# Kernel optimization log

Measured on AMD Instinct MI355X. Metric: run time of the kernel, lower is better.

## Reference

```python
import jax, jax.numpy as jnp
import numpy as np

N, E, D, H = 50000, 500000, 128, 4
FH = D // H  # per-head dim of gat1
NEG_SLOPE = 0.2
EPS = 1e-16  # PyG softmax denominator epsilon


def _gat_layer(x, src, dst, W, a_src, a_dst, bias, heads, fh):
    # W: [D_in, heads*fh]; a_src/a_dst: [heads, fh]; bias: [heads*fh]
    n = x.shape[0]
    xp = (x @ W).reshape(n, heads, fh)                     # [N,H,F]
    alpha_s = jnp.einsum('nhf,hf->nh', xp, a_src)          # [N,H]
    alpha_d = jnp.einsum('nhf,hf->nh', xp, a_dst)
    e = alpha_s[src] + alpha_d[dst]                        # [E,H]
    e = jnp.where(e > 0, e, NEG_SLOPE * e)                 # leaky_relu
    # edge softmax grouped by destination node
    m = jax.lax.stop_gradient(jax.ops.segment_max(e, dst, num_segments=n))
    a = jnp.exp(e - m[dst])
    denom = jax.ops.segment_sum(a, dst, num_segments=n)
    a = a / (denom[dst] + EPS)                             # [E,H]
    msg = a[:, :, None] * xp[src]                          # [E,H,F]
    out = jax.ops.segment_sum(msg, dst, num_segments=n)    # [N,H,F]
    return out.reshape(n, heads * fh) + bias


def setup_inputs() -> dict:
    key = jax.random.key(0)
    ks = jax.random.split(key, 20)

    def glorot(k, shape):
        fan_in, fan_out = shape[0], shape[-1]
        std = (2.0 / (fan_in + fan_out)) ** 0.5
        return std * jax.random.normal(k, shape, dtype=jnp.float32)

    inp = {
        'x': jax.random.normal(ks[0], (N, 1), dtype=jnp.float32),
        'edge_index': jax.random.randint(ks[1], (E, 2), 0, N, dtype=jnp.int64 if jax.config.jax_enable_x64 else jnp.int32),
        'W_emb': glorot(ks[2], (1, D)),   # nn.Linear(1, d_node), stored as [in,out]
        'b_emb': jnp.zeros((D,), jnp.float32),
        # gat1: in=D, heads=H, per-head out=FH
        'W1': glorot(ks[3], (D, H * FH)),
        'as1': glorot(ks[4], (H, FH)),
        'ad1': glorot(ks[5], (H, FH)),
        'b1': jnp.zeros((H * FH,), jnp.float32),
        # gat2/3/4: in=D, heads=1, out=D
        'W2': glorot(ks[6], (D, D)), 'as2': glorot(ks[7], (1, D)), 'ad2': glorot(ks[8], (1, D)), 'b2': jnp.zeros((D,), jnp.float32),
        'W3': glorot(ks[9], (D, D)), 'as3': glorot(ks[10], (1, D)), 'ad3': glorot(ks[11], (1, D)), 'b3': jnp.zeros((D,), jnp.float32),
        'W4': glorot(ks[12], (D, D)), 'as4': glorot(ks[13], (1, D)), 'ad4': glorot(ks[14], (1, D)), 'b4': jnp.zeros((D,), jnp.float32),
    }
    return inp


def reference(x, edge_index, W_emb, b_emb, W1, as1, ad1, b1,
              W2, as2, ad2, b2, W3, as3, ad3, b3, W4, as4, ad4, b4):
    # emb: Linear(1 -> D)
    h = x @ W_emb + b_emb                                  # [N,D]
    # edge_index.t(): row 0 = src, row 1 = dst; GATConv adds self-loops
    loop = jnp.arange(N, dtype=edge_index.dtype)
    src = jnp.concatenate([edge_index[:, 0], loop])
    dst = jnp.concatenate([edge_index[:, 1], loop])
    h = jax.nn.relu(_gat_layer(h, src, dst, W1, as1, ad1, b1, H, FH))
    h = jax.nn.relu(_gat_layer(h, src, dst, W2, as2, ad2, b2, 1, D))
    h = jax.nn.relu(_gat_layer(h, src, dst, W3, as3, ad3, b3, 1, D))
    h = _gat_layer(h, src, dst, W4, as4, ad4, b4, 1, D)
    return h
```

## Files before the change

kernel.cpp:

```cpp
#include <hip/hip_runtime.h>
#include <math.h>


#define LEAKY(e) ((e) > 0.f ? (e) : 0.2f * (e))

typedef __attribute__((ext_vector_type(8))) short bf16x8;
typedef __attribute__((ext_vector_type(4))) float f32x4;

__device__ inline ushort f32_to_bf16_rne(float f) {
    unsigned u = __float_as_uint(f);
    unsigned r = (u + 0x7FFFu + ((u >> 16) & 1u)) >> 16;
    return (ushort)r;
}
__device__ inline float bf16_to_f32(ushort h) { return __uint_as_float((unsigned)h << 16); }
__device__ inline unsigned pack2(float a, float b) {
    return (unsigned)f32_to_bf16_rne(a) | ((unsigned)f32_to_bf16_rne(b) << 16);
}


__global__ void k_scatterpad(const int* __restrict__ ei, int E, int N,
                             int* __restrict__ deg, int* __restrict__ csr_pad,
                             int* __restrict__ ovf_cnt, int2* __restrict__ ovf,
                             int ovf_cap) {
    int e = blockIdx.x * blockDim.x + threadIdx.x;
    int Et = E + N;
    if (e >= Et) return;
    int src, dst;
    if (e < E) { int2 p = ((const int2*)ei)[e]; src = p.x; dst = p.y; }
    else { src = dst = e - E; }
    int pos = atomicAdd(&deg[dst], 1);
    if (pos < 64) {
        csr_pad[(dst << 6) + pos] = src;
    } else {
        int o = atomicAdd(ovf_cnt, 1);
        if (o < ovf_cap) ovf[o] = make_int2(dst, src);
    }
}


__global__ void k_prep(const float* __restrict__ Wa, const float* __restrict__ Wb,
                       const float* __restrict__ Wc,
                       const float* __restrict__ asa, const float* __restrict__ asb,
                       const float* __restrict__ asc,
                       const float* __restrict__ ada, const float* __restrict__ adb,
                       const float* __restrict__ adc,
                       const float* __restrict__ W_emb, const float* __restrict__ b_emb,
                       const float* __restrict__ W1g, const float* __restrict__ as1g,
                       const float* __restrict__ ad1g,
                       ushort* __restrict__ hi0, ushort* __restrict__ lo0,
                       ushort* __restrict__ hi1, ushort* __restrict__ lo1,
                       ushort* __restrict__ hi2, ushort* __restrict__ lo2,
                       float* __restrict__ was0, float* __restrict__ was1,
                       float* __restrict__ was2,
                       float* __restrict__ wad0, float* __restrict__ wad1,
                       float* __restrict__ wad2,
                       float* __restrict__ consts) {
    __shared__ float su[128], sv[128];
    int b = blockIdx.x, tid = threadIdx.x;
    if (b < 192) {
        int l = b >> 6;
        int idx = (b & 63) * 256 + tid;
        const float* W = (l == 0) ? Wa : (l == 1) ? Wb : Wc;
        ushort* ph = (l == 0) ? hi0 : (l == 1) ? hi1 : hi2;
        ushort* pl = (l == 0) ? lo0 : (l == 1) ? lo1 : lo2;
        int k = idx >> 7, c = idx & 127;
        float w = W[idx];
        ushort hi = f32_to_bf16_rne(w);
        ushort lo = f32_to_bf16_rne(w - bf16_to_f32(hi));
        ph[c * 128 + k] = hi;
        pl[c * 128 + k] = lo;
    } else if (b < 195) {
        if (tid >= 128) return;
        int l = b - 192;
        const float* W  = (l == 0) ? Wa : (l == 1) ? Wb : Wc;
        const float* av = (l == 0) ? asa : (l == 1) ? asb : asc;
        const float* dv = (l == 0) ? ada : (l == 1) ? adb : adc;
        float* ws = (l == 0) ? was0 : (l == 1) ? was1 : was2;
        float* wd = (l == 0) ? wad0 : (l == 1) ? wad1 : wad2;
        int k = tid;
        float s = 0.f, d = 0.f;
        for (int c = 0; c < 128; c++) {
            float w = W[k * 128 + c];
            s += w * av[c];
            d += w * dv[c];
        }
        ws[k] = s; wd[k] = d;
    } else {
        if (tid >= 128) return;
        int f = tid;
        float u = 0.f, v = 0.f;
        for (int k = 0; k < 128; k++) {
            u += W_emb[k] * W1g[k * 128 + f];
            v += b_emb[k] * W1g[k * 128 + f];
        }
        su[f] = u; sv[f] = v;
        consts[f] = u; consts[128 + f] = v;
        __syncthreads();
        if (f < 4) {
            float P = 0.f, Q = 0.f, R = 0.f, S = 0.f;
            for (int j = 0; j < 32; j++) {
                float uu = su[f * 32 + j], vv = sv[f * 32 + j];
                float a = as1g[f * 32 + j], d = ad1g[f * 32 + j];
                P += uu * a; Q += vv * a; R += uu * d; S += vv * d;
            }
            consts[256 + f] = P; consts[260 + f] = Q;
            consts[264 + f] = R; consts[268 + f] = S;
        }
    }
}

__global__ __launch_bounds__(256) void k_l1(const float* __restrict__ x,
        const int* __restrict__ deg, const int* __restrict__ csr_pad,
        const int* __restrict__ ovf_cnt, const int2* __restrict__ ovf,
        const float* __restrict__ consts, const float* __restrict__ b1,
        const float* __restrict__ was2, const float* __restrict__ wad2,
        float* __restrict__ hout, float* __restrict__ a_s, float* __restrict__ a_d, int n) {
    __shared__ float sm[64][4], smw[64][4];
    int tid = threadIdx.x;
    int nl = tid >> 2, q = tid & 3;
    int node = blockIdx.x * 64 + nl;
    bool valid = node < n;
    float P = consts[256 + q], Q = consts[260 + q];
    float R = consts[264 + q], Sc = consts[268 + q];
    float den = 0.f, S = 0.f;
    if (valid) {
        float xd = x[node];
        float c0 = xd * R + Sc + Q;
        int dg = deg[node];
        int dlim = min(dg, 64);
        for (int i = 0; i < dlim; i++) {
            float xs = x[csr_pad[(node << 6) + i]];
            float e = xs * P + c0;
            e = LEAKY(e);
            float w = __expf(e);
            den += w;
            S += w * xs;
        }
        if (dg > 64) {
            int no = *ovf_cnt;
            for (int i = 0; i < no; i++) {
                int2 p = ovf[i];
                if (p.x == node) {
                    float xs = x[p.y];
                    float e = xs * P + c0;
                    e = LEAKY(e);
                    float w = __expf(e);
                    den += w;
                    S += w * xs;
                }
            }
        }
    }
    float inv = 1.f / (den + 1e-16f);
    sm[nl][q] = S * inv;
    smw[nl][q] = den * inv;
    __syncthreads();
    float Sn = sm[nl][q], Swn = smw[nl][q];
    float ps = 0.f, pd = 0.f;
    if (valid) {
#pragma unroll
        for (int j = 0; j < 8; j++) {
            int f = q * 32 + j * 4;
            float4 u = *(const float4*)(consts + f);
            float4 v = *(const float4*)(consts + 128 + f);
            float4 b = *(const float4*)(b1 + f);
            float4 ws = *(const float4*)(was2 + f);
            float4 wd = *(const float4*)(wad2 + f);
            float4 val;
            val.x = fmaxf(Sn * u.x + Swn * v.x + b.x, 0.f);
            val.y = fmaxf(Sn * u.y + Swn * v.y + b.y, 0.f);
            val.z = fmaxf(Sn * u.z + Swn * v.z + b.z, 0.f);
            val.w = fmaxf(Sn * u.w + Swn * v.w + b.w, 0.f);
            *(float4*)(hout + (size_t)node * 128 + f) = val;
            ps += val.x * ws.x + val.y * ws.y + val.z * ws.z + val.w * ws.w;
            pd += val.x * wd.x + val.y * wd.y + val.z * wd.z + val.w * wd.w;
        }
    }
    ps += __shfl_xor(ps, 1, 64); ps += __shfl_xor(ps, 2, 64);
    pd += __shfl_xor(pd, 1, 64); pd += __shfl_xor(pd, 2, 64);
    if (q == 0 && valid) { a_s[node] = ps; a_d[node] = pd; }
}

__global__ __launch_bounds__(256) void k_aggh(const float* __restrict__ h,
        const float* __restrict__ as, const float* __restrict__ ad,
        const int* __restrict__ deg, const int* __restrict__ csr_pad,
        const int* __restrict__ ovf_cnt, const int2* __restrict__ ovf,
        unsigned* __restrict__ aggp, int n) {
    __shared__ int2 s_sw[4][64];
    int w = threadIdx.x >> 6, lane = threadIdx.x & 63;
    int node = blockIdx.x * 4 + w;
    if (node >= n) return;
    int dg = deg[node];
    float adval = ad[node];
    const char* hbase = (const char*)h;

    if (dg <= 64) {
        int boff = 0;
        float e = -INFINITY;
        if (lane < dg) {
            int src = csr_pad[(node << 6) + lane];
            boff = src << 9;
            e = LEAKY(as[src] + adval);
        }
        float m = e;
#pragma unroll
        for (int off = 32; off > 0; off >>= 1) m = fmaxf(m, __shfl_xor(m, off, 64));
        float wt = (lane < dg) ? __expf(e - m) : 0.f;
        float den = wt;
#pragma unroll
        for (int off = 32; off > 0; off >>= 1) den += __shfl_xor(den, off, 64);
        s_sw[w][lane] = make_int2(boff, __float_as_int(wt));
        __builtin_amdgcn_wave_barrier();

        int half = lane >> 5;
        int q16 = (lane & 31) * 16;
        float4 acc = make_float4(0.f, 0.f, 0.f, 0.f);
        int degp = (dg + 7) & ~7;
        for (int j = 0; j < degp; j += 8) {
#pragma unroll
            for (int t = 0; t < 4; t++) {
                int2 p = s_sw[w][j + 2 * t + half];
                float4 v = *(const float4*)(hbase + p.x + q16);
                float wt2 = __int_as_float(p.y);
                acc.x += wt2 * v.x; acc.y += wt2 * v.y;
                acc.z += wt2 * v.z; acc.w += wt2 * v.w;
            }
        }
        acc.x += __shfl_xor(acc.x, 32, 64);
        acc.y += __shfl_xor(acc.y, 32, 64);
        acc.z += __shfl_xor(acc.z, 32, 64);
        acc.w += __shfl_xor(acc.w, 32, 64);
        float inv = 1.f / (den + 1e-16f);
        if (lane < 32) {
            float o0 = acc.x * inv, o1 = acc.y * inv;
            float o2 = acc.z * inv, o3 = acc.w * inv;
            ushort h0 = f32_to_bf16_rne(o0), h1 = f32_to_bf16_rne(o1);
            ushort h2 = f32_to_bf16_rne(o2), h3 = f32_to_bf16_rne(o3);
            uint4 pk;
            pk.x = (unsigned)h0 | ((unsigned)h1 << 16);
            pk.y = pack2(o0 - bf16_to_f32(h0), o1 - bf16_to_f32(h1));
            pk.z = (unsigned)h2 | ((unsigned)h3 << 16);
            pk.w = pack2(o2 - bf16_to_f32(h2), o3 - bf16_to_f32(h3));
            ((uint4*)aggp)[(size_t)node * 32 + lane] = pk;
        }
    } else {
        int lane8 = lane * 8;
        int no = *ovf_cnt;
        int psrc = csr_pad[(node << 6) + lane];
        float m = LEAKY(as[psrc] + adval);
        for (int i = lane; i < no; i += 64) {
            int2 p = ovf[i];
            if (p.x == node) m = fmaxf(m, LEAKY(as[p.y] + adval));
        }
#pragma unroll
        for (int off = 32; off > 0; off >>= 1) m = fmaxf(m, __shfl_xor(m, off, 64));
        float den = 0.f;
        float2 acc = make_float2(0.f, 0.f);
        for (int i = 0; i < 64; i++) {
            int src = csr_pad[(node << 6) + i];
            float e = LEAKY(as[src] + adval);
            float wt = __expf(e - m);
            den += wt;
            float2 v = *(const float2*)(hbase + ((size_t)src << 9) + lane8);
            acc.x += wt * v.x; acc.y += wt * v.y;
        }
        for (int i = 0; i < no; i++) {
            int2 p = ovf[i];
            if (p.x == node) {
                float e = LEAKY(as[p.y] + adval);
                float wt = __expf(e - m);
                den += wt;
                float2 v = *(const float2*)(hbase + ((size_t)p.y << 9) + lane8);
                acc.x += wt * v.x; acc.y += wt * v.y;
            }
        }
        float inv = 1.f / (den + 1e-16f);
        float o0 = acc.x * inv, o1 = acc.y * inv;
        ushort h0 = f32_to_bf16_rne(o0), h1 = f32_to_bf16_rne(o1);
        ((uint2*)aggp)[(size_t)node * 64 + lane] =
            make_uint2((unsigned)h0 | ((unsigned)h1 << 16),
                       pack2(o0 - bf16_to_f32(h0), o1 - bf16_to_f32(h1)));
    }
}

__global__ __launch_bounds__(512) void k_gemm(const uint2* __restrict__ aggp,
        const ushort* __restrict__ wt_hi, const ushort* __restrict__ wt_lo,
        const float* __restrict__ bias, float* __restrict__ hout,
        const float* __restrict__ was_nx, const float* __restrict__ wad_nx,
        float* __restrict__ as_nx, float* __restrict__ ad_nx,
        int n, int do_relu) {
    __shared__ ushort Bh[16 * 128 * 8];
    __shared__ ushort Bl[16 * 128 * 8];
    int tid = threadIdx.x;
#pragma unroll
    for (int rep = 0; rep < 4; rep++) {
        int c = rep * 512 + tid;
        int col = c >> 4, kc = c & 15;
        *(uint4*)(Bh + (size_t)(kc * 128 + col) * 8) = *(const uint4*)(wt_hi + (size_t)col * 128 + kc * 8);
        *(uint4*)(Bl + (size_t)(kc * 128 + col) * 8) = *(const uint4*)(wt_lo + (size_t)col * 128 + kc * 8);
    }
    __syncthreads();

    int wid = tid >> 6, lane = tid & 63;
    int lrow = lane & 15, kgrp = lane >> 4;
    int row_base = blockIdx.x * 128 + wid * 16;

    f32x4 acc[8];
#pragma unroll
    for (int nn = 0; nn < 8; nn++) { acc[nn][0] = 0.f; acc[nn][1] = 0.f; acc[nn][2] = 0.f; acc[nn][3] = 0.f; }

#pragma unroll
    for (int ks = 0; ks < 4; ks++) {
        int kbase = ks * 32 + kgrp * 8;
        int arow = min(row_base + lrow, n - 1);
        const uint2* ap = aggp + (size_t)arow * 64 + (kbase >> 1);
        uint4 q0 = *(const uint4*)ap;
        uint4 q1 = *(const uint4*)(ap + 2);
        int4 hi4 = make_int4(q0.x, q0.z, q1.x, q1.z);
        int4 lo4 = make_int4(q0.y, q0.w, q1.y, q1.w);
        bf16x8 ah = *(bf16x8*)&hi4;
        bf16x8 al = *(bf16x8*)&lo4;
        int kc = ks * 4 + kgrp;
#pragma unroll
        for (int nn = 0; nn < 8; nn++) {
            int col = nn * 16 + lrow;
            bf16x8 bh = *(const bf16x8*)(Bh + (size_t)(kc * 128 + col) * 8);
            bf16x8 bl = *(const bf16x8*)(Bl + (size_t)(kc * 128 + col) * 8);
            acc[nn] = __builtin_amdgcn_mfma_f32_16x16x32_bf16(ah, bh, acc[nn], 0, 0, 0);
            acc[nn] = __builtin_amdgcn_mfma_f32_16x16x32_bf16(ah, bl, acc[nn], 0, 0, 0);
            acc[nn] = __builtin_amdgcn_mfma_f32_16x16x32_bf16(al, bh, acc[nn], 0, 0, 0);
        }
    }

    float bv[8], wsv[8], wdv[8];
#pragma unroll
    for (int nn = 0; nn < 8; nn++) bv[nn] = bias[nn * 16 + lrow];
    if (was_nx) {
#pragma unroll
        for (int nn = 0; nn < 8; nn++) {
            wsv[nn] = was_nx[nn * 16 + lrow];
            wdv[nn] = wad_nx[nn * 16 + lrow];
        }
    }

#pragma unroll
    for (int i = 0; i < 4; i++) {
        int row = row_base + kgrp * 4 + i;
        if (row < n) {
            float ps = 0.f, pd = 0.f;
#pragma unroll
            for (int nn = 0; nn < 8; nn++) {
                float val = acc[nn][i] + bv[nn];
                if (do_relu) val = fmaxf(val, 0.f);
                hout[(size_t)row * 128 + nn * 16 + lrow] = val;
                if (was_nx) { ps += val * wsv[nn]; pd += val * wdv[nn]; }
            }
            if (was_nx) {
#pragma unroll
                for (int off = 1; off < 16; off <<= 1) {
                    ps += __shfl_xor(ps, off, 16);
                    pd += __shfl_xor(pd, off, 16);
                }
                if (lrow == 0) { as_nx[row] = ps; ad_nx[row] = pd; }
            }
        }
    }
}


extern "C" void kernel_launch(void* const* d_in, const int* in_sizes, int n_in,
                              void* d_out, int out_size, void* d_ws, size_t ws_size,
                              hipStream_t stream) {
    const float* x     = (const float*)d_in[0];
    const int*   ei    = (const int*)d_in[1];
    const float* W_emb = (const float*)d_in[2];
    const float* b_emb = (const float*)d_in[3];
    const float* W1g   = (const float*)d_in[4];
    const float* as1g  = (const float*)d_in[5];
    const float* ad1g  = (const float*)d_in[6];
    const float* b1    = (const float*)d_in[7];
    const float* Wl[3]  = {(const float*)d_in[8],  (const float*)d_in[12], (const float*)d_in[16]};
    const float* asl[3] = {(const float*)d_in[9],  (const float*)d_in[13], (const float*)d_in[17]};
    const float* adl[3] = {(const float*)d_in[10], (const float*)d_in[14], (const float*)d_in[18]};
    const float* bl[3]  = {(const float*)d_in[11], (const float*)d_in[15], (const float*)d_in[19]};
    float* out = (float*)d_out;

    int N = in_sizes[0];
    int E = in_sizes[1] / 2;
    int Et = E + N;
    const int OVF_CAP = 65536;

    char* ws = (char*)d_ws;
    size_t off = 0;
    auto alloc = [&](size_t bytes) { size_t p = off; off += (bytes + 255) & ~(size_t)255; return p; };
    int*   deg      = (int*)(ws + alloc((size_t)N * 4));
    int*   ovf_cnt  = (int*)(ws + alloc(4));
    int2*  ovf      = (int2*)(ws + alloc((size_t)OVF_CAP * 8));
    int*   csr_pad  = (int*)(ws + alloc((size_t)N * 64 * 4));
    float* consts   = (float*)(ws + alloc(272 * 4));
    float* a_s0     = (float*)(ws + alloc((size_t)N * 4));
    float* a_d0     = (float*)(ws + alloc((size_t)N * 4));
    float* a_s1     = (float*)(ws + alloc((size_t)N * 4));
    float* a_d1     = (float*)(ws + alloc((size_t)N * 4));
    float* hA       = (float*)(ws + alloc((size_t)N * 128 * 4));
    unsigned* aggp  = (unsigned*)(ws + alloc((size_t)N * 64 * 8));
    ushort* wt_hi[3]; ushort* wt_lo[3];
    float* was[3]; float* wad[3];
    for (int l = 0; l < 3; l++) {
        wt_hi[l] = (ushort*)(ws + alloc(128 * 128 * 2));
        wt_lo[l] = (ushort*)(ws + alloc(128 * 128 * 2));
        was[l]   = (float*)(ws + alloc(128 * 4));
        wad[l]   = (float*)(ws + alloc(128 * 4));
    }

    hipMemsetAsync(deg, 0, (size_t)N * 4, stream);
    hipMemsetAsync(ovf_cnt, 0, 4, stream);
    k_scatterpad<<<(Et + 255) / 256, 256, 0, stream>>>(ei, E, N, deg, csr_pad,
                                                       ovf_cnt, ovf, OVF_CAP);
    k_prep<<<196, 256, 0, stream>>>(Wl[0], Wl[1], Wl[2], asl[0], asl[1], asl[2],
                                    adl[0], adl[1], adl[2],
                                    W_emb, b_emb, W1g, as1g, ad1g,
                                    wt_hi[0], wt_lo[0], wt_hi[1], wt_lo[1], wt_hi[2], wt_lo[2],
                                    was[0], was[1], was[2], wad[0], wad[1], wad[2],
                                    consts);

    k_l1<<<(N + 63) / 64, 256, 0, stream>>>(x, deg, csr_pad, ovf_cnt, ovf, consts, b1,
                                            was[0], wad[0], hA, a_s0, a_d0, N);

    float* as_cur = a_s0; float* ad_cur = a_d0;
    float* as_nxt = a_s1; float* ad_nxt = a_d1;
    for (int l = 0; l < 3; l++) {
        k_aggh<<<(N + 3) / 4, 256, 0, stream>>>(hA, as_cur, ad_cur, deg, csr_pad,
                                                ovf_cnt, ovf, aggp, N);
        if (l < 2) {
            k_gemm<<<(N + 127) / 128, 512, 0, stream>>>((const uint2*)aggp, wt_hi[l], wt_lo[l], bl[l], hA,
                                                        was[l + 1], wad[l + 1], as_nxt, ad_nxt, N, 1);
            float* t;
            t = as_cur; as_cur = as_nxt; as_nxt = t;
            t = ad_cur; ad_cur = ad_nxt; ad_nxt = t;
        } else {
            k_gemm<<<(N + 127) / 128, 512, 0, stream>>>((const uint2*)aggp, wt_hi[l], wt_lo[l], bl[l], out,
                                                        nullptr, nullptr, nullptr, nullptr, N, 0);
        }
    }
}
```

Baseline: 247.7 us.

## Parallelize layer-1 edges across a wavefront, prefetch GEMM A, merge overflow counter

k_l1 now assigns one 64-lane wavefront per node, with 16 lanes per head striding over edges and shuffle reductions. It replaces the old scheme where one thread per head looped serially over every edge. The GEMM kernel issues its A-operand global loads into registers before the LDS barrier, so they overlap with the weight staging. The overflow counter is folded into deg[N], which removes one memset. The trade-offs are more shuffle reductions per node and higher register pressure in the GEMM.

```diff
diff --git a/kernel.cpp b/kernel.cpp
--- a/kernel.cpp
+++ b/kernel.cpp
@@ -20,8 +20,7 @@
 
 __global__ void k_scatterpad(const int* __restrict__ ei, int E, int N,
                              int* __restrict__ deg, int* __restrict__ csr_pad,
-                             int* __restrict__ ovf_cnt, int2* __restrict__ ovf,
-                             int ovf_cap) {
+                             int2* __restrict__ ovf, int ovf_cap) {
     int e = blockIdx.x * blockDim.x + threadIdx.x;
     int Et = E + N;
     if (e >= Et) return;
@@ -32,7 +31,7 @@
     if (pos < 64) {
         csr_pad[(dst << 6) + pos] = src;
     } else {
-        int o = atomicAdd(ovf_cnt, 1);
+        int o = atomicAdd(&deg[N], 1);
         if (o < ovf_cap) ovf[o] = make_int2(dst, src);
     }
 }
@@ -111,80 +110,75 @@
 
 __global__ __launch_bounds__(256) void k_l1(const float* __restrict__ x,
         const int* __restrict__ deg, const int* __restrict__ csr_pad,
-        const int* __restrict__ ovf_cnt, const int2* __restrict__ ovf,
+        const int2* __restrict__ ovf,
         const float* __restrict__ consts, const float* __restrict__ b1,
         const float* __restrict__ was2, const float* __restrict__ wad2,
-        float* __restrict__ hout, float* __restrict__ a_s, float* __restrict__ a_d, int n) {
-    __shared__ float sm[64][4], smw[64][4];
-    int tid = threadIdx.x;
-    int nl = tid >> 2, q = tid & 3;
-    int node = blockIdx.x * 64 + nl;
-    bool valid = node < n;
+        float* __restrict__ hout, float* __restrict__ a_s, float* __restrict__ a_d,
+        int n) {
+    int w = threadIdx.x >> 6, lane = threadIdx.x & 63;
+    int node = blockIdx.x * 4 + w;
+    if (node >= n) return;
+    int q = lane & 3;
+    int el = lane >> 2;
     float P = consts[256 + q], Q = consts[260 + q];
     float R = consts[264 + q], Sc = consts[268 + q];
+    float xd = x[node];
+    float c0 = xd * R + Sc + Q;
+    int dg = deg[node];
+    int dlim = min(dg, 64);
     float den = 0.f, S = 0.f;
-    if (valid) {
-        float xd = x[node];
-        float c0 = xd * R + Sc + Q;
-        int dg = deg[node];
-        int dlim = min(dg, 64);
-        for (int i = 0; i < dlim; i++) {
-            float xs = x[csr_pad[(node << 6) + i]];
-            float e = xs * P + c0;
-            e = LEAKY(e);
-            float w = __expf(e);
-            den += w;
-            S += w * xs;
-        }
-        if (dg > 64) {
-            int no = *ovf_cnt;
-            for (int i = 0; i < no; i++) {
-                int2 p = ovf[i];
-                if (p.x == node) {
-                    float xs = x[p.y];
-                    float e = xs * P + c0;
-                    e = LEAKY(e);
-                    float w = __expf(e);
-                    den += w;
-                    S += w * xs;
-                }
-            }
-        }
+    for (int i = el; i < dlim; i += 16) {
+        float xs = x[csr_pad[(node << 6) + i]];
+        float e = xs * P + c0;
+        e = LEAKY(e);
+        float wgt = __expf(e);
+        den += wgt;
+        S += wgt * xs;
+    }
+    if (dg > 64) {
+        int no = deg[n];
+        for (int i = el; i < no; i += 16) {
+            int2 p = ovf[i];
+            if (p.x == node) {
+                float xs = x[p.y];
+                float e = xs * P + c0;
+                e = LEAKY(e);
+                float wgt = __expf(e);
+                den += wgt;
+                S += wgt * xs;
+            }
+        }
+    }
+#pragma unroll
+    for (int off = 4; off < 64; off <<= 1) {
+        den += __shfl_xor(den, off, 64);
+        S += __shfl_xor(S, off, 64);
     }
     float inv = 1.f / (den + 1e-16f);
-    sm[nl][q] = S * inv;
-    smw[nl][q] = den * inv;
-    __syncthreads();
-    float Sn = sm[nl][q], Swn = smw[nl][q];
-    float ps = 0.f, pd = 0.f;
-    if (valid) {
-#pragma unroll
-        for (int j = 0; j < 8; j++) {
-            int f = q * 32 + j * 4;
-            float4 u = *(const float4*)(consts + f);
-            float4 v = *(const float4*)(consts + 128 + f);
-            float4 b = *(const float4*)(b1 + f);
-            float4 ws = *(const float4*)(was2 + f);
-            float4 wd = *(const float4*)(wad2 + f);
-            float4 val;
-            val.x = fmaxf(Sn * u.x + Swn * v.x + b.x, 0.f);
-            val.y = fmaxf(Sn * u.y + Swn * v.y + b.y, 0.f);
-            val.z = fmaxf(Sn * u.z + Swn * v.z + b.z, 0.f);
-            val.w = fmaxf(Sn * u.w + Swn * v.w + b.w, 0.f);
-            *(float4*)(hout + (size_t)node * 128 + f) = val;
-            ps += val.x * ws.x + val.y * ws.y + val.z * ws.z + val.w * ws.w;
-            pd += val.x * wd.x + val.y * wd.y + val.z * wd.z + val.w * wd.w;
-        }
-    }
-    ps += __shfl_xor(ps, 1, 64); ps += __shfl_xor(ps, 2, 64);
-    pd += __shfl_xor(pd, 1, 64); pd += __shfl_xor(pd, 2, 64);
-    if (q == 0 && valid) { a_s[node] = ps; a_d[node] = pd; }
+    float Sn = S * inv, Swn = den * inv;
+    int f = q * 32 + el * 2;
+    float2 u  = *(const float2*)(consts + f);
+    float2 v  = *(const float2*)(consts + 128 + f);
+    float2 bb = *(const float2*)(b1 + f);
+    float2 ws = *(const float2*)(was2 + f);
+    float2 wd = *(const float2*)(wad2 + f);
+    float v0 = fmaxf(Sn * u.x + Swn * v.x + bb.x, 0.f);
+    float v1 = fmaxf(Sn * u.y + Swn * v.y + bb.y, 0.f);
+    *(float2*)(hout + (size_t)node * 128 + f) = make_float2(v0, v1);
+    float ps = v0 * ws.x + v1 * ws.y;
+    float pd = v0 * wd.x + v1 * wd.y;
+#pragma unroll
+    for (int off = 1; off < 64; off <<= 1) {
+        ps += __shfl_xor(ps, off, 64);
+        pd += __shfl_xor(pd, off, 64);
+    }
+    if (lane == 0) { a_s[node] = ps; a_d[node] = pd; }
 }
 
 __global__ __launch_bounds__(256) void k_aggh(const float* __restrict__ h,
         const float* __restrict__ as, const float* __restrict__ ad,
         const int* __restrict__ deg, const int* __restrict__ csr_pad,
-        const int* __restrict__ ovf_cnt, const int2* __restrict__ ovf,
+        const int2* __restrict__ ovf,
         unsigned* __restrict__ aggp, int n) {
     __shared__ int2 s_sw[4][64];
     int w = threadIdx.x >> 6, lane = threadIdx.x & 63;
@@ -245,7 +239,7 @@
         }
     } else {
         int lane8 = lane * 8;
-        int no = *ovf_cnt;
+        int no = deg[n];
         int psrc = csr_pad[(node << 6) + lane];
         float m = LEAKY(as[psrc] + adval);
         for (int i = lane; i < no; i += 64) {
@@ -299,11 +293,20 @@
         *(uint4*)(Bh + (size_t)(kc * 128 + col) * 8) = *(const uint4*)(wt_hi + (size_t)col * 128 + kc * 8);
         *(uint4*)(Bl + (size_t)(kc * 128 + col) * 8) = *(const uint4*)(wt_lo + (size_t)col * 128 + kc * 8);
     }
-    __syncthreads();
 
     int wid = tid >> 6, lane = tid & 63;
     int lrow = lane & 15, kgrp = lane >> 4;
     int row_base = blockIdx.x * 128 + wid * 16;
+    int arow = min(row_base + lrow, n - 1);
+
+    const uint4* ap = (const uint4*)(aggp + (size_t)arow * 64);
+    uint4 qa[8];
+#pragma unroll
+    for (int ks = 0; ks < 4; ks++) {
+        qa[2 * ks]     = ap[ks * 8 + kgrp * 2];
+        qa[2 * ks + 1] = ap[ks * 8 + kgrp * 2 + 1];
+    }
+    __syncthreads();
 
     f32x4 acc[8];
 #pragma unroll
@@ -311,11 +314,7 @@
 
 #pragma unroll
     for (int ks = 0; ks < 4; ks++) {
-        int kbase = ks * 32 + kgrp * 8;
-        int arow = min(row_base + lrow, n - 1);
-        const uint2* ap = aggp + (size_t)arow * 64 + (kbase >> 1);
-        uint4 q0 = *(const uint4*)ap;
-        uint4 q1 = *(const uint4*)(ap + 2);
+        uint4 q0 = qa[2 * ks], q1 = qa[2 * ks + 1];
         int4 hi4 = make_int4(q0.x, q0.z, q1.x, q1.z);
         int4 lo4 = make_int4(q0.y, q0.w, q1.y, q1.w);
         bf16x8 ah = *(bf16x8*)&hi4;
@@ -393,8 +392,7 @@
     char* ws = (char*)d_ws;
     size_t off = 0;
     auto alloc = [&](size_t bytes) { size_t p = off; off += (bytes + 255) & ~(size_t)255; return p; };
-    int*   deg      = (int*)(ws + alloc((size_t)N * 4));
-    int*   ovf_cnt  = (int*)(ws + alloc(4));
+    int*   deg      = (int*)(ws + alloc((size_t)(N + 1) * 4));
     int2*  ovf      = (int2*)(ws + alloc((size_t)OVF_CAP * 8));
     int*   csr_pad  = (int*)(ws + alloc((size_t)N * 64 * 4));
     float* consts   = (float*)(ws + alloc(272 * 4));
@@ -413,10 +411,9 @@
         wad[l]   = (float*)(ws + alloc(128 * 4));
     }
 
-    hipMemsetAsync(deg, 0, (size_t)N * 4, stream);
-    hipMemsetAsync(ovf_cnt, 0, 4, stream);
+    hipMemsetAsync(deg, 0, (size_t)(N + 1) * 4, stream);
     k_scatterpad<<<(Et + 255) / 256, 256, 0, stream>>>(ei, E, N, deg, csr_pad,
-                                                       ovf_cnt, ovf, OVF_CAP);
+                                                       ovf, OVF_CAP);
     k_prep<<<196, 256, 0, stream>>>(Wl[0], Wl[1], Wl[2], asl[0], asl[1], asl[2],
                                     adl[0], adl[1], adl[2],
                                     W_emb, b_emb, W1g, as1g, ad1g,
@@ -424,14 +421,14 @@
                                     was[0], was[1], was[2], wad[0], wad[1], wad[2],
                                     consts);
 
-    k_l1<<<(N + 63) / 64, 256, 0, stream>>>(x, deg, csr_pad, ovf_cnt, ovf, consts, b1,
-                                            was[0], wad[0], hA, a_s0, a_d0, N);
+    k_l1<<<(N + 3) / 4, 256, 0, stream>>>(x, deg, csr_pad, ovf, consts, b1,
+                                          was[0], wad[0], hA, a_s0, a_d0, N);
 
     float* as_cur = a_s0; float* ad_cur = a_d0;
     float* as_nxt = a_s1; float* ad_nxt = a_d1;
     for (int l = 0; l < 3; l++) {
         k_aggh<<<(N + 3) / 4, 256, 0, stream>>>(hA, as_cur, ad_cur, deg, csr_pad,
-                                                ovf_cnt, ovf, aggp, N);
+                                                ovf, aggp, N);
         if (l < 2) {
             k_gemm<<<(N + 127) / 128, 512, 0, stream>>>((const uint2*)aggp, wt_hi[l], wt_lo[l], bl[l], hA,
                                                         was[l + 1], wad[l + 1], as_nxt, ad_nxt, N, 1);
```

Result: no change. 247.4 us (-0.2%).
